# Kernel optimization log

Hardware: AMD Instinct MI355X
Metric: run time of the kernel (lower is better)

The kernel has to match this reference:

```python
import jax, jax.numpy as jnp
import numpy as np

NEG_BIG = -9e15
ALPHA = 0.2  # LeakyReLU negative slope


def setup_inputs() -> dict:
    key = jax.random.key(0)
    k1, k2, k3, k4 = jax.random.split(key, 4)
    B, N, Fin, Fout = 4, 2048, 128, 128
    h = jax.random.normal(k1, (B, N, Fin), dtype=jnp.float32)
    adj = jax.random.randint(k2, (N, N), 0, 2, dtype=jnp.int32)
    W = jax.random.normal(k3, (Fin, Fout), dtype=jnp.float32) * 0.1
    a = jax.random.normal(k4, (2 * Fout, 1), dtype=jnp.float32) * 0.1
    return {"h": h, "adj": adj, "W": W, "a": a}


def reference(h, adj, W, a):
    # Wh: [B, N, Fout]
    Wh = jnp.einsum('bnf,fo->bno', h, W)
    Fout = W.shape[1]
    a1 = a[:Fout, 0]   # attends to source i
    a2 = a[Fout:, 0]   # attends to target j
    # Decomposed form of leakyrelu(cat([Wh_i, Wh_j]) @ a):
    # e_ij = leakyrelu(a1.Wh_i + a2.Wh_j)  -> [B, N, N]
    f1 = Wh @ a1  # [B, N]
    f2 = Wh @ a2  # [B, N]
    e = jax.nn.leaky_relu(f1[:, :, None] + f2[:, None, :], negative_slope=ALPHA)
    attention = jnp.where(adj[None, :, :] > 0, e, jnp.float32(NEG_BIG))
    attention = jax.nn.softmax(attention, axis=2)
    # dropout is identity in eval mode
    h_prime = jnp.einsum('bij,bjo->bio', attention, Wh)
    return h_prime
```

## Files before the change

### kernel.cpp

```cpp
#include <hip/hip_runtime.h>

#define BB 4
#define NN 2048
#define FF 128
#define NP 2176
#define ALPHA 0.2f
#define SHIFT_C 16.0f

typedef short bf16x8 __attribute__((ext_vector_type(8)));
typedef float f32x4 __attribute__((ext_vector_type(4)));
typedef unsigned u32;

__device__ inline short f2bf(float f) {
    union { float f; unsigned u; } v; v.f = f;
    unsigned r = (v.u + 0x7FFFu + ((v.u >> 16) & 1u)) >> 16;
    return (short)r;
}
__device__ inline float bf2f(short s) {
    union { float f; unsigned u; } v;
    v.u = ((unsigned)(unsigned short)s) << 16;
    return v.f;
}

__global__ __launch_bounds__(256) void k_wh(const float* __restrict__ h,
                                            const float* __restrict__ W,
                                            const float* __restrict__ a,
                                            const int* __restrict__ adj,
                                            short* __restrict__ WhHiT,
                                            short* __restrict__ WhLoT,
                                            float* __restrict__ f1,
                                            float* __restrict__ f2,
                                            u32* __restrict__ adjp) {
    __shared__ float Wa[2 * FF];
    __shared__ float hs[16 * 132];
    int tid = threadIdx.x;
    int r0 = blockIdx.x * 16;

    {
        int fin = tid & 127;
        const float* av = (tid < 128) ? a : (a + FF);
        const float* wr = W + (size_t)fin * FF;
        float s = 0.f;
        for (int o = 0; o < FF; o += 4) {
            float4 wv = *(const float4*)(wr + o);
            float4 avv = *(const float4*)(av + o);
            s += wv.x * avv.x + wv.y * avv.y + wv.z * avv.z + wv.w * avv.w;
        }
        Wa[(tid < 128 ? 0 : FF) + fin] = s;
    }
    {
        const float4* src = (const float4*)(h + (size_t)r0 * FF);
        float4* dst = (float4*)hs;
        dst[tid] = src[tid];
        dst[256 + tid] = src[256 + tid];
    }
    {
        int g = blockIdx.x * 256 + tid;
        int row = g >> 6, wd = g & 63;
        const int4* ar = (const int4*)(adj + (size_t)row * NN + wd * 32);
        u32 word = 0;
#pragma unroll
        for (int q = 0; q < 8; ++q) {
            int4 v = ar[q];
            word |= (u32)(v.x > 0) << (q * 4);
            word |= (u32)(v.y > 0) << (q * 4 + 1);
            word |= (u32)(v.z > 0) << (q * 4 + 2);
            word |= (u32)(v.w > 0) << (q * 4 + 3);
        }
        adjp[row * 64 + wd] = word;
    }
    __syncthreads();

    {
        int w = tid >> 6, lane = tid & 63;
        float wa1_0 = Wa[lane], wa1_1 = Wa[lane + 64];
        float wa2_0 = Wa[FF + lane], wa2_1 = Wa[FF + lane + 64];
        for (int rr = 0; rr < 4; ++rr) {
            int rloc = w * 4 + rr;
            int row = r0 + rloc;
            float x0 = hs[rloc * FF + lane], x1 = hs[rloc * FF + lane + 64];
            float s1 = x0 * wa1_0 + x1 * wa1_1;
            float s2 = x0 * wa2_0 + x1 * wa2_1;
#pragma unroll
            for (int m = 32; m >= 1; m >>= 1) {
                s1 += __shfl_xor(s1, m, 64);
                s2 += __shfl_xor(s2, m, 64);
            }
            if (lane == 0) { f1[row] = s1; f2[row] = s2; }
        }
    }

    int f4 = (tid & 31) * 4;
    int rg = tid >> 5;
    float acc[2][4];
#pragma unroll
    for (int rr = 0; rr < 2; ++rr)
#pragma unroll
        for (int cc = 0; cc < 4; ++cc) acc[rr][cc] = 0.f;

    for (int k0 = 0; k0 < FF; k0 += 4) {
        float4 wv[4];
#pragma unroll
        for (int kk = 0; kk < 4; ++kk)
            wv[kk] = *(const float4*)(W + (size_t)(k0 + kk) * FF + f4);
        float4 hv[2];
#pragma unroll
        for (int rr = 0; rr < 2; ++rr)
            hv[rr] = *(const float4*)(hs + (rg * 2 + rr) * FF + k0);
#pragma unroll
        for (int rr = 0; rr < 2; ++rr) {
            float hk[4] = {hv[rr].x, hv[rr].y, hv[rr].z, hv[rr].w};
#pragma unroll
            for (int kk = 0; kk < 4; ++kk) {
                acc[rr][0] += hk[kk] * wv[kk].x;
                acc[rr][1] += hk[kk] * wv[kk].y;
                acc[rr][2] += hk[kk] * wv[kk].z;
                acc[rr][3] += hk[kk] * wv[kk].w;
            }
        }
    }

    __syncthreads();
    {
#pragma unroll
        for (int rr = 0; rr < 2; ++rr)
            *(float4*)(hs + (rg * 2 + rr) * 132 + f4) =
                make_float4(acc[rr][0], acc[rr][1], acc[rr][2], acc[rr][3]);
    }
    __syncthreads();
    {
        int fo = tid >> 1, jh = tid & 1;
        bf16x8 hv_, lv_;
#pragma unroll
        for (int jj = 0; jj < 8; ++jj) {
            float v = hs[(jh * 8 + jj) * 132 + fo];
            short hh = f2bf(v);
            hv_[jj] = hh;
            lv_[jj] = f2bf(v - bf2f(hh));
        }
        int b = r0 >> 11;
        int j0 = (r0 & (NN - 1)) + jh * 8;
        size_t off = (size_t)(b * FF + fo) * NP + j0;
        *(bf16x8*)(WhHiT + off) = hv_;
        *(bf16x8*)(WhLoT + off) = lv_;
    }
}

#define EV(f2v, f1v, wv, bi) ({ float _t = (f1v) + (f2v); float _x = fmaxf(_t, ALPHA * _t); \
    __expf(_x - SHIFT_C) * (float)(((wv) >> (bi)) & 1u); })

#define BUILD_A(Adst, F1V, WV, SP) { \
    float pa, pb; \
    pa = EV(q0.x, F1V, WV, bb + 0); pb = EV(q0.y, F1V, WV, bb + 1); \
    SP += pa + pb; \
    asm("v_cvt_pk_bf16_f32 %0, %1, %2" : "=v"(Adst.u[0]) : "v"(pa), "v"(pb)); \
    pa = EV(q0.z, F1V, WV, bb + 2); pb = EV(q0.w, F1V, WV, bb + 3); \
    SP += pa + pb; \
    asm("v_cvt_pk_bf16_f32 %0, %1, %2" : "=v"(Adst.u[1]) : "v"(pa), "v"(pb)); \
    pa = EV(q1.x, F1V, WV, bb + 4); pb = EV(q1.y, F1V, WV, bb + 5); \
    SP += pa + pb; \
    asm("v_cvt_pk_bf16_f32 %0, %1, %2" : "=v"(Adst.u[2]) : "v"(pa), "v"(pb)); \
    pa = EV(q1.z, F1V, WV, bb + 6); pb = EV(q1.w, F1V, WV, bb + 7); \
    SP += pa + pb; \
    asm("v_cvt_pk_bf16_f32 %0, %1, %2" : "=v"(Adst.u[3]) : "v"(pa), "v"(pb)); }

__global__ __launch_bounds__(512) void k_attn(const short* __restrict__ WhHiT,
                                              const short* __restrict__ WhLoT,
                                              const u32* __restrict__ adjp,
                                              const float* __restrict__ f1,
                                              const float* __restrict__ f2,
                                              float* __restrict__ out) {
    __shared__ __align__(16) char lds[35072];
    float* row_ps = (float*)(lds + 32768);
    float* row_inv = (float*)(lds + 34816);

    int tid = threadIdx.x;
    int w = tid >> 6, lane = tid & 63;
    int blk = blockIdx.x;
    int b = blk >> 8;
    int tile = (blk >> 3) & 31;
    int oc = blk & 7;
    int i0 = tile * 64;

    int r_c = lane & 15, kg = lane >> 4;

    const float* f2b = f2 + b * NN;
    float f1m[4];
#pragma unroll
    for (int mi = 0; mi < 4; ++mi)
        f1m[mi] = f1[b * NN + i0 + mi * 16 + r_c];
    const u32* ap0 = adjp + (size_t)(i0 + r_c) * 64;

    const ptrdiff_t dLo = (ptrdiff_t)BB * FF * NP;
    int s0 = w * 8;
    const short* pB0 = WhHiT + (size_t)(b * FF + oc * 16 + r_c) * NP + s0 * 32 + kg * 8;

    f32x4 acc0 = {0,0,0,0}, acc1 = {0,0,0,0}, acc2 = {0,0,0,0}, acc3 = {0,0,0,0};
    float sp0 = 0.f, sp1 = 0.f, sp2 = 0.f, sp3 = 0.f;

#pragma unroll
    for (int s8 = 0; s8 < 8; ++s8) {
        int s = s0 + s8;
        float4 q0 = *(const float4*)(f2b + s * 32 + kg * 8);
        float4 q1 = *(const float4*)(f2b + s * 32 + kg * 8 + 4);
        u32 w0 = ap0[s], w1 = ap0[1024 + s], w2 = ap0[2048 + s], w3 = ap0[3072 + s];
        bf16x8 bh = *(const bf16x8*)(pB0);
        bf16x8 bl = *(const bf16x8*)(pB0 + dLo);

        int bb = kg * 8;
        {
            union { u32 u[4]; bf16x8 v; } A;
            BUILD_A(A, f1m[0], w0, sp0)
            acc0 = __builtin_amdgcn_mfma_f32_16x16x32_bf16(A.v, bh, acc0, 0, 0, 0);
            acc0 = __builtin_amdgcn_mfma_f32_16x16x32_bf16(A.v, bl, acc0, 0, 0, 0);
        }
        {
            union { u32 u[4]; bf16x8 v; } A;
            BUILD_A(A, f1m[1], w1, sp1)
            acc1 = __builtin_amdgcn_mfma_f32_16x16x32_bf16(A.v, bh, acc1, 0, 0, 0);
            acc1 = __builtin_amdgcn_mfma_f32_16x16x32_bf16(A.v, bl, acc1, 0, 0, 0);
        }
        {
            union { u32 u[4]; bf16x8 v; } A;
            BUILD_A(A, f1m[2], w2, sp2)
            acc2 = __builtin_amdgcn_mfma_f32_16x16x32_bf16(A.v, bh, acc2, 0, 0, 0);
            acc2 = __builtin_amdgcn_mfma_f32_16x16x32_bf16(A.v, bl, acc2, 0, 0, 0);
        }
        {
            union { u32 u[4]; bf16x8 v; } A;
            BUILD_A(A, f1m[3], w3, sp3)
            acc3 = __builtin_amdgcn_mfma_f32_16x16x32_bf16(A.v, bh, acc3, 0, 0, 0);
            acc3 = __builtin_amdgcn_mfma_f32_16x16x32_bf16(A.v, bl, acc3, 0, 0, 0);
        }

        pB0 += 32;
    }

    sp0 += __shfl_xor(sp0, 16, 64); sp0 += __shfl_xor(sp0, 32, 64);
    sp1 += __shfl_xor(sp1, 16, 64); sp1 += __shfl_xor(sp1, 32, 64);
    sp2 += __shfl_xor(sp2, 16, 64); sp2 += __shfl_xor(sp2, 32, 64);
    sp3 += __shfl_xor(sp3, 16, 64); sp3 += __shfl_xor(sp3, 32, 64);
    if (lane < 16) {
        row_ps[w * 64 + lane]      = sp0;
        row_ps[w * 64 + 16 + lane] = sp1;
        row_ps[w * 64 + 32 + lane] = sp2;
        row_ps[w * 64 + 48 + lane] = sp3;
    }
    {
        char* img = lds + w * 4096;
#define STACC(MI, A) { int ch = (r_c * 16 + (MI) * 4 + kg) ^ (r_c & 7); \
                       *(f32x4*)(img + ch * 16) = (A); }
        STACC(0, acc0) STACC(1, acc1) STACC(2, acc2) STACC(3, acc3)
#undef STACC
    }
    __syncthreads();
    if (tid < 64) {
        float t = 0.f;
#pragma unroll
        for (int ww = 0; ww < 8; ++ww) t += row_ps[ww * 64 + tid];
        row_inv[tid] = 1.0f / t;
    }
    __syncthreads();

    if (lane < 32) {
        int colg = w * 2 + (lane >> 4);
        int rq = lane & 15;
        int ch = (colg * 16 + rq) ^ (colg & 7);
        f32x4 v = {0, 0, 0, 0};
#pragma unroll
        for (int im = 0; im < 8; ++im)
            v += *(const f32x4*)(lds + im * 4096 + ch * 16);
        f32x4 rinv = *(const f32x4*)((char*)row_inv + rq * 16);
        float* ob = out + ((size_t)b * NN + i0 + rq * 4) * FF + oc * 16 + colg;
#pragma unroll
        for (int q = 0; q < 4; ++q)
            ob[(size_t)q * FF] = v[q] * rinv[q];
    }
}

extern "C" void kernel_launch(void* const* d_in, const int* in_sizes, int n_in,
                              void* d_out, int out_size, void* d_ws, size_t ws_size,
                              hipStream_t stream) {
    const float* h   = (const float*)d_in[0];
    const int*   adj = (const int*)d_in[1];
    const float* W   = (const float*)d_in[2];
    const float* a   = (const float*)d_in[3];
    float* out = (float*)d_out;

    short* WhHiT = (short*)d_ws;
    short* WhLoT = WhHiT + (size_t)BB * FF * NP;
    float* f1 = (float*)(WhLoT + (size_t)BB * FF * NP);
    float* f2 = f1 + (size_t)BB * NN;
    u32* adjp = (u32*)(f2 + (size_t)BB * NN);

    k_wh<<<(BB * NN) / 16, 256, 0, stream>>>(h, W, a, adj, WhHiT, WhLoT, f1, f2, adjp);
    k_attn<<<1024, 512, 0, stream>>>(WhHiT, WhLoT, adjp, f1, f2, out);
}
```

Before: 140.0 us.

## Retile attention kernel to 32 rows by 32 output columns per block

Each block now covers 32 query rows and 32 output features instead of 64 rows and 16 features, keeping the same block count. This halves how often the exp/leakyrelu attention weights are recomputed per output element: they are now built for 4 column groups rather than 8. In exchange, each B-operand load is reused by fewer rows and twice as much Wh data is loaded per block. The LDS reduction layout and output indexing are rewritten to match.

```diff
diff --git a/kernel.cpp b/kernel.cpp
--- a/kernel.cpp
+++ b/kernel.cpp
@@ -170,108 +170,97 @@
                                               const float* __restrict__ f1,
                                               const float* __restrict__ f2,
                                               float* __restrict__ out) {
-    __shared__ __align__(16) char lds[35072];
+    __shared__ __align__(16) char lds[33920];
     float* row_ps = (float*)(lds + 32768);
-    float* row_inv = (float*)(lds + 34816);
+    float* row_inv = (float*)(lds + 33792);
 
     int tid = threadIdx.x;
     int w = tid >> 6, lane = tid & 63;
     int blk = blockIdx.x;
     int b = blk >> 8;
-    int tile = (blk >> 3) & 31;
-    int oc = blk & 7;
-    int i0 = tile * 64;
+    int tile = (blk >> 2) & 63;
+    int qt = blk & 3;
+    int i0 = tile * 32;
 
     int r_c = lane & 15, kg = lane >> 4;
 
     const float* f2b = f2 + b * NN;
-    float f1m[4];
-#pragma unroll
-    for (int mi = 0; mi < 4; ++mi)
-        f1m[mi] = f1[b * NN + i0 + mi * 16 + r_c];
+    float f10 = f1[b * NN + i0 + r_c];
+    float f11 = f1[b * NN + i0 + 16 + r_c];
     const u32* ap0 = adjp + (size_t)(i0 + r_c) * 64;
 
     const ptrdiff_t dLo = (ptrdiff_t)BB * FF * NP;
     int s0 = w * 8;
-    const short* pB0 = WhHiT + (size_t)(b * FF + oc * 16 + r_c) * NP + s0 * 32 + kg * 8;
-
-    f32x4 acc0 = {0,0,0,0}, acc1 = {0,0,0,0}, acc2 = {0,0,0,0}, acc3 = {0,0,0,0};
-    float sp0 = 0.f, sp1 = 0.f, sp2 = 0.f, sp3 = 0.f;
+    const short* pB0 = WhHiT + (size_t)(b * FF + qt * 32 + 0 * 16 + r_c) * NP + s0 * 32 + kg * 8;
+    const short* pB1 = WhHiT + (size_t)(b * FF + qt * 32 + 1 * 16 + r_c) * NP + s0 * 32 + kg * 8;
+
+    f32x4 acc0_0 = {0,0,0,0}, acc0_1 = {0,0,0,0};
+    f32x4 acc1_0 = {0,0,0,0}, acc1_1 = {0,0,0,0};
+    float sp0 = 0.f, sp1 = 0.f;
 
 #pragma unroll
     for (int s8 = 0; s8 < 8; ++s8) {
         int s = s0 + s8;
         float4 q0 = *(const float4*)(f2b + s * 32 + kg * 8);
         float4 q1 = *(const float4*)(f2b + s * 32 + kg * 8 + 4);
-        u32 w0 = ap0[s], w1 = ap0[1024 + s], w2 = ap0[2048 + s], w3 = ap0[3072 + s];
-        bf16x8 bh = *(const bf16x8*)(pB0);
-        bf16x8 bl = *(const bf16x8*)(pB0 + dLo);
+        u32 w0 = ap0[s], w1 = ap0[1024 + s];
+        bf16x8 bh0 = *(const bf16x8*)(pB0); bf16x8 bl0 = *(const bf16x8*)(pB0 + dLo);
+        bf16x8 bh1 = *(const bf16x8*)(pB1); bf16x8 bl1 = *(const bf16x8*)(pB1 + dLo);
 
         int bb = kg * 8;
         {
             union { u32 u[4]; bf16x8 v; } A;
-            BUILD_A(A, f1m[0], w0, sp0)
-            acc0 = __builtin_amdgcn_mfma_f32_16x16x32_bf16(A.v, bh, acc0, 0, 0, 0);
-            acc0 = __builtin_amdgcn_mfma_f32_16x16x32_bf16(A.v, bl, acc0, 0, 0, 0);
+            BUILD_A(A, f10, w0, sp0)
+            acc0_0 = __builtin_amdgcn_mfma_f32_16x16x32_bf16(A.v, bh0, acc0_0, 0, 0, 0);
+            acc0_0 = __builtin_amdgcn_mfma_f32_16x16x32_bf16(A.v, bl0, acc0_0, 0, 0, 0);
+            acc1_0 = __builtin_amdgcn_mfma_f32_16x16x32_bf16(A.v, bh1, acc1_0, 0, 0, 0);
+            acc1_0 = __builtin_amdgcn_mfma_f32_16x16x32_bf16(A.v, bl1, acc1_0, 0, 0, 0);
         }
         {
             union { u32 u[4]; bf16x8 v; } A;
-            BUILD_A(A, f1m[1], w1, sp1)
-            acc1 = __builtin_amdgcn_mfma_f32_16x16x32_bf16(A.v, bh, acc1, 0, 0, 0);
-            acc1 = __builtin_amdgcn_mfma_f32_16x16x32_bf16(A.v, bl, acc1, 0, 0, 0);
-        }
-        {
-            union { u32 u[4]; bf16x8 v; } A;
-            BUILD_A(A, f1m[2], w2, sp2)
-            acc2 = __builtin_amdgcn_mfma_f32_16x16x32_bf16(A.v, bh, acc2, 0, 0, 0);
-            acc2 = __builtin_amdgcn_mfma_f32_16x16x32_bf16(A.v, bl, acc2, 0, 0, 0);
-        }
-        {
-            union { u32 u[4]; bf16x8 v; } A;
-            BUILD_A(A, f1m[3], w3, sp3)
-            acc3 = __builtin_amdgcn_mfma_f32_16x16x32_bf16(A.v, bh, acc3, 0, 0, 0);
-            acc3 = __builtin_amdgcn_mfma_f32_16x16x32_bf16(A.v, bl, acc3, 0, 0, 0);
-        }
-
-        pB0 += 32;
+            BUILD_A(A, f11, w1, sp1)
+            acc0_1 = __builtin_amdgcn_mfma_f32_16x16x32_bf16(A.v, bh0, acc0_1, 0, 0, 0);
+            acc0_1 = __builtin_amdgcn_mfma_f32_16x16x32_bf16(A.v, bl0, acc0_1, 0, 0, 0);
+            acc1_1 = __builtin_amdgcn_mfma_f32_16x16x32_bf16(A.v, bh1, acc1_1, 0, 0, 0);
+            acc1_1 = __builtin_amdgcn_mfma_f32_16x16x32_bf16(A.v, bl1, acc1_1, 0, 0, 0);
+        }
+
+        pB0 += 32; pB1 += 32;
     }
 
     sp0 += __shfl_xor(sp0, 16, 64); sp0 += __shfl_xor(sp0, 32, 64);
     sp1 += __shfl_xor(sp1, 16, 64); sp1 += __shfl_xor(sp1, 32, 64);
-    sp2 += __shfl_xor(sp2, 16, 64); sp2 += __shfl_xor(sp2, 32, 64);
-    sp3 += __shfl_xor(sp3, 16, 64); sp3 += __shfl_xor(sp3, 32, 64);
     if (lane < 16) {
-        row_ps[w * 64 + lane]      = sp0;
-        row_ps[w * 64 + 16 + lane] = sp1;
-        row_ps[w * 64 + 32 + lane] = sp2;
-        row_ps[w * 64 + 48 + lane] = sp3;
+        row_ps[w * 32 + lane] = sp0;
+        row_ps[w * 32 + 16 + lane] = sp1;
     }
     {
         char* img = lds + w * 4096;
-#define STACC(MI, A) { int ch = (r_c * 16 + (MI) * 4 + kg) ^ (r_c & 7); \
-                       *(f32x4*)(img + ch * 16) = (A); }
-        STACC(0, acc0) STACC(1, acc1) STACC(2, acc2) STACC(3, acc3)
+#define STACC(NI, MI, A) { int ch = (((NI)*16 + r_c) * 8 + (MI)*4 + kg) ^ (r_c & 7); \
+                           *(f32x4*)(img + ch * 16) = (A); }
+        STACC(0, 0, acc0_0) STACC(0, 1, acc0_1)
+        STACC(1, 0, acc1_0) STACC(1, 1, acc1_1)
 #undef STACC
     }
     __syncthreads();
-    if (tid < 64) {
+    if (tid < 32) {
         float t = 0.f;
 #pragma unroll
-        for (int ww = 0; ww < 8; ++ww) t += row_ps[ww * 64 + tid];
+        for (int ww = 0; ww < 8; ++ww) t += row_ps[ww * 32 + tid];
         row_inv[tid] = 1.0f / t;
     }
     __syncthreads();
 
     if (lane < 32) {
-        int colg = w * 2 + (lane >> 4);
-        int rq = lane & 15;
-        int ch = (colg * 16 + rq) ^ (colg & 7);
+        int colg = w * 4 + (lane >> 3);
+        int rq = lane & 7;
+        int ch = (colg * 8 + rq) ^ (colg & 7);
         f32x4 v = {0, 0, 0, 0};
 #pragma unroll
         for (int im = 0; im < 8; ++im)
             v += *(const f32x4*)(lds + im * 4096 + ch * 16);
         f32x4 rinv = *(const f32x4*)((char*)row_inv + rq * 16);
-        float* ob = out + ((size_t)b * NN + i0 + rq * 4) * FF + oc * 16 + colg;
+        float* ob = out + ((size_t)b * NN + i0 + rq * 4) * FF + qt * 32 + colg;
 #pragma unroll
         for (int q = 0; q < 4; ++q)
             ob[(size_t)q * FF] = v[q] * rinv[q];
```

Result: faster. 129.9 us (-7.2%).
